# Optimization experiments

Measured on AMD Instinct MI355X. Metric: run time of the kernel, lower is better.

Reference implementation:

```python
import jax, jax.numpy as jnp
import numpy as np

S, L = 512, 32            # number of sequences, max sequence length
IN_FEATURES = 13824       # 512*3*3 + 1024*3*3 ROI features
HID = 1024                # Head.hidden_dim
LSTM_H = HID // 2         # per-direction hidden size (bidirectional)
N_CLASSES = 4787
BN_EPS = 1e-5


def _make_ragged():
    lengths = (4 + (np.arange(S) % 29)).astype(np.int32)  # 4..32, sum = 9121
    n = int(lengths.sum())
    perm = np.random.RandomState(0).permutation(n).astype(np.int32)
    seq_idx = np.zeros((S, L), dtype=np.int32)
    off = 0
    for i, l in enumerate(lengths):
        seq_idx[i, :l] = perm[off:off + l]
        off += l
    return n, jnp.asarray(seq_idx), jnp.asarray(lengths)


def setup_inputs() -> dict:
    n, seq_idx, lengths = _make_ragged()
    key = jax.random.key(0)
    ks = jax.random.split(key, 16)
    w = lambda k, shp, s=0.02: (jax.random.normal(k, shp, dtype=jnp.float32) * s)
    return {
        "x": jax.random.normal(ks[0], (n, IN_FEATURES), dtype=jnp.float32),
        "fc1_w": w(ks[1], (HID, IN_FEATURES)),
        "fc1_b": w(ks[2], (HID,)),
        "bn_gamma": jnp.ones((HID,), jnp.float32),
        "bn_beta": jnp.zeros((HID,), jnp.float32),
        "fc2_w": w(ks[3], (N_CLASSES, HID)),
        "fc2_b": w(ks[4], (N_CLASSES,)),
        "w_ih_f": w(ks[5], (4 * LSTM_H, HID)),
        "w_hh_f": w(ks[6], (4 * LSTM_H, LSTM_H)),
        "b_ih_f": w(ks[7], (4 * LSTM_H,)),
        "b_hh_f": w(ks[8], (4 * LSTM_H,)),
        "w_ih_b": w(ks[9], (4 * LSTM_H, HID)),
        "w_hh_b": w(ks[10], (4 * LSTM_H, LSTM_H)),
        "b_ih_b": w(ks[11], (4 * LSTM_H,)),
        "b_hh_b": w(ks[12], (4 * LSTM_H,)),
        "seq_idx": seq_idx,
        "lengths": lengths,
    }


def _lstm_scan(seq_x, w_ih, w_hh, b_ih, b_hh):
    # seq_x: [S, L, HID] -> outputs [S, L, LSTM_H]; PyTorch gate order i,f,g,o
    s = seq_x.shape[0]
    h0 = jnp.zeros((s, LSTM_H), seq_x.dtype)
    c0 = jnp.zeros((s, LSTM_H), seq_x.dtype)
    x_gates = jnp.einsum('slh,gh->slg', seq_x, w_ih) + b_ih + b_hh  # precompute input gates

    def step(carry, xg):
        h, c = carry
        g = xg + h @ w_hh.T
        i, f, gg, o = jnp.split(g, 4, axis=-1)
        c = jax.nn.sigmoid(f) * c + jax.nn.sigmoid(i) * jnp.tanh(gg)
        h = jax.nn.sigmoid(o) * jnp.tanh(c)
        return (h, c), h

    _, hs = jax.lax.scan(step, (h0, c0), x_gates.transpose(1, 0, 2))  # [L, S, H]
    return hs.transpose(1, 0, 2)


def reference(x, fc1_w, fc1_b, bn_gamma, bn_beta, fc2_w, fc2_b,
              w_ih_f, w_hh_f, b_ih_f, b_hh_f,
              w_ih_b, w_hh_b, b_ih_b, b_hh_b,
              seq_idx, lengths):
    n = x.shape[0]
    # Head: fc1 -> relu -> BatchNorm1d (training-mode batch stats)
    h = jax.nn.relu(x @ fc1_w.T + fc1_b)
    mean = h.mean(axis=0)
    var = jnp.mean((h - mean) ** 2, axis=0)
    feats = (h - mean) * jax.lax.rsqrt(var + BN_EPS) * bn_gamma + bn_beta  # [N, HID]

    # ragged gather into packed [S, L, HID]
    mask = jnp.arange(L)[None, :] < lengths[:, None]          # [S, L]
    gidx = jnp.where(mask, seq_idx, 0)
    seq_x = feats[gidx] * mask[:, :, None]                    # zero padded slots

    # forward direction (padding at tail: harmless to causal scan)
    hf = _lstm_scan(seq_x, w_ih_f, w_hh_f, b_ih_f, b_hh_f)
    # backward direction: reverse each sequence within its valid length
    rev = jnp.clip(lengths[:, None] - 1 - jnp.arange(L)[None, :], 0, L - 1)  # [S, L]
    seq_rev = jnp.take_along_axis(seq_x, rev[:, :, None], axis=1)
    hb_rev = _lstm_scan(seq_rev, w_ih_b, w_hh_b, b_ih_b, b_hh_b)
    hb = jnp.take_along_axis(hb_rev, rev[:, :, None], axis=1)  # un-reverse (involution on valid region)

    out = jnp.concatenate([hf, hb], axis=-1)                   # [S, L, HID]

    # scatter back to flat roi order; padded slots dropped out-of-bounds
    sidx = jnp.where(mask, seq_idx, n).reshape(-1)
    lstm_feats = jnp.zeros((n, HID), feats.dtype).at[sidx].set(
        out.reshape(-1, HID), mode='drop')

    logits = lstm_feats @ fc2_w.T + fc2_b                      # apply_fc_out
    return logits
```

## Files before the change

kernel.cpp:

```cpp
#include <hip/hip_runtime.h>

typedef short short8v __attribute__((ext_vector_type(8)));
typedef float f32x4 __attribute__((ext_vector_type(4)));
typedef _Float16 h4v __attribute__((ext_vector_type(4)));

__device__ __forceinline__ unsigned short f2bf(float f){
  unsigned int u = __float_as_uint(f);
  u += 0x7fffu + ((u >> 16) & 1u);
  return (unsigned short)(u >> 16);
}
__device__ __forceinline__ float bf2f(unsigned short h){
  return __uint_as_float(((unsigned int)h) << 16);
}
union H2F { unsigned short u; _Float16 h; };
__device__ __forceinline__ float fp16f(unsigned short b){ H2F t; t.u = b; return (float)t.h; }

typedef __attribute__((address_space(1))) const unsigned int gu32;
typedef __attribute__((address_space(3))) unsigned int lu32;
__device__ __forceinline__ void gl16(const void* g, void* l){
  __builtin_amdgcn_global_load_lds((gu32*)g, (lu32*)l, 16, 0, 0);
}

template<int EPI>
__global__ __launch_bounds__(512, 2)
void gemm256(const unsigned short* __restrict__ A, const unsigned short* __restrict__ B,
             void* __restrict__ Cout, int M, int N, int K, int lda, int ldb, int ldc,
             const float* __restrict__ bias)
{
  __shared__ __align__(16) unsigned short As[2 * 2 * 256 * 32];
  __shared__ __align__(16) unsigned short Bs[2 * 2 * 256 * 32];

  const int tid = threadIdx.x;
  const int gx = gridDim.x;
  const int nwg = gx * gridDim.y;
  int dd = blockIdx.y * gx + blockIdx.x;
  int q8 = nwg >> 3, r8 = nwg & 7, xc = dd & 7, t8 = dd >> 3;
  int Lid = (xc < r8 ? xc * (q8 + 1) : r8 * (q8 + 1) + (xc - r8) * q8) + t8;
  const int bcol = (Lid % gx) * 256;
  const int brow = (Lid / gx) * 256;

  const int l = tid & 63, w = tid >> 6;
  const int wr = w >> 2;
  const int wn = w & 3;
  const int r16 = l & 15, kg = l >> 4;
  const int swz = (r16 >> 1) & 3;
  const int srow4 = l >> 2, sblk = l & 3;
  const int scol = (sblk ^ ((l >> 3) & 3)) * 8;

  const int kz = blockIdx.z * K;
  const unsigned short* Ag = A + (size_t)(brow + w * 32 + srow4) * lda + kz + scol;
  const unsigned short* Bg = B + (size_t)(bcol + w * 32 + srow4) * ldb + kz + scol;
  unsigned short* Asd = As + w * 1024;
  unsigned short* Bsd = Bs + w * 1024;

#define STA(buf, kh, kt) do { \
    gl16(Ag + (size_t)(kt) * 64 + (kh) * 32, Asd + (buf) * 16384 + (kh) * 8192); \
    gl16(Ag + (size_t)(kt) * 64 + (kh) * 32 + (size_t)16 * lda, Asd + (buf) * 16384 + (kh) * 8192 + 512); \
  } while (0)
#define STB(buf, kh, kt) do { \
    gl16(Bg + (size_t)(kt) * 64 + (kh) * 32, Bsd + (buf) * 16384 + (kh) * 8192); \
    gl16(Bg + (size_t)(kt) * 64 + (kh) * 32 + (size_t)16 * ldb, Bsd + (buf) * 16384 + (kh) * 8192 + 512); \
  } while (0)

  const unsigned short* Ard = As + (wr * 128 + r16) * 32 + ((kg ^ swz) * 8);
  const unsigned short* Brd = Bs + (wn * 64 + r16) * 32 + ((kg ^ swz) * 8);

  f32x4 acc[8][4];
  #pragma unroll
  for (int m = 0; m < 8; m++)
    #pragma unroll
    for (int nn = 0; nn < 4; nn++) { f32x4 z = {0.f, 0.f, 0.f, 0.f}; acc[m][nn] = z; }

  short8v af[4], bfr[4];

#define LDA4(c, kk, mq) { \
    _Pragma("unroll") for (int i = 0; i < 4; i++) \
      af[i] = *(const short8v*)(Ard + (c) * 16384 + (kk) * 8192 + ((mq) * 4 + i) * 512); }
#define LDB4(c, kk) { \
    _Pragma("unroll") for (int nn = 0; nn < 4; nn++) \
      bfr[nn] = *(const short8v*)(Brd + (c) * 16384 + (kk) * 8192 + nn * 512); }
#define MFMAQ(mq) { \
    __builtin_amdgcn_s_setprio(1); \
    _Pragma("unroll") for (int i = 0; i < 4; i++) { \
      _Pragma("unroll") for (int nn = 0; nn < 4; nn++) \
        acc[(mq) * 4 + i][nn] = __builtin_amdgcn_mfma_f32_16x16x32_bf16(af[i], bfr[nn], acc[(mq) * 4 + i][nn], 0, 0, 0); \
    } \
    __builtin_amdgcn_s_setprio(0); }

  const int nk = K >> 6;
  STA(0, 0, 0); STB(0, 0, 0); STA(0, 1, 0); STB(0, 1, 0);
  asm volatile("s_waitcnt vmcnt(4)" ::: "memory");
  __builtin_amdgcn_s_barrier();
  __builtin_amdgcn_sched_barrier(0);

  for (int j = 0; j < nk; j++) {
    const int c = j & 1, nb = c ^ 1;
    const bool pf = (j + 1 < nk);
    LDB4(c, 0); LDA4(c, 0, 0);
    if (pf) STA(nb, 0, j + 1);
    __builtin_amdgcn_s_barrier();
    MFMAQ(0);
    __builtin_amdgcn_s_barrier();
    LDA4(c, 0, 1);
    if (pf) STB(nb, 0, j + 1);
    __builtin_amdgcn_s_barrier();
    MFMAQ(1);
    if (pf) asm volatile("s_waitcnt vmcnt(4)" ::: "memory");
    else    asm volatile("s_waitcnt vmcnt(0)" ::: "memory");
    __builtin_amdgcn_s_barrier();
    __builtin_amdgcn_sched_barrier(0);
    LDB4(c, 1); LDA4(c, 1, 0);
    if (pf) STA(nb, 1, j + 1);
    __builtin_amdgcn_s_barrier();
    MFMAQ(0);
    __builtin_amdgcn_s_barrier();
    LDA4(c, 1, 1);
    if (pf) STB(nb, 1, j + 1);
    __builtin_amdgcn_s_barrier();
    MFMAQ(1);
    if (pf) asm volatile("s_waitcnt vmcnt(4)" ::: "memory");
    __builtin_amdgcn_s_barrier();
    __builtin_amdgcn_sched_barrier(0);
  }
#undef STA
#undef STB
#undef LDA4
#undef LDB4
#undef MFMAQ

  #pragma unroll
  for (int m = 0; m < 8; m++) {
    const int row0 = brow + wr * 128 + m * 16 + kg * 4;
    #pragma unroll
    for (int nn = 0; nn < 4; nn++) {
      const int col = bcol + wn * 64 + nn * 16 + r16;
      if (col < N) {
        const float bv = (EPI == 5) ? 0.f : bias[col];
        #pragma unroll
        for (int rr = 0; rr < 4; rr++) {
          const int row = row0 + rr;
          if (row < M) {
            float val = acc[m][nn][rr] + bv;
            if (EPI == 3) {
              int dL = col >> 11, rc = col & 2047;
              int cg = rc >> 6, g = (rc >> 4) & 3, u = rc & 15;
              int pc = (dL << 11) + (((cg << 4) + u) << 2) + g;
              ((_Float16*)Cout)[(size_t)row * ldc + pc] = (_Float16)val;
            } else if (EPI == 5) {
              ((_Float16*)Cout)[(size_t)blockIdx.z * M * ldc + (size_t)row * ldc + col] = (_Float16)val;
            } else {
              ((float*)Cout)[(size_t)row * ldc + col] = val;
            }
          }
        }
      }
    }
  }
}

__global__ __launch_bounds__(256) void fc1_reduce(const _Float16* __restrict__ P, const float* __restrict__ bias,
                                                  unsigned short* __restrict__ h, float* __restrict__ part,
                                                  int n, int mpad) {
  int b = blockIdx.x, tid = threadIdx.x;
  int c0 = tid * 4;
  float4 bsv = *(const float4*)(bias + c0);
  float s[4] = {0,0,0,0}, qq[4] = {0,0,0,0};
  int rbeg = b * 32;
  for (int r = rbeg; r < rbeg + 32; r++) {
    h4v a0 = *(const h4v*)(P + (size_t)r * 1024 + c0);
    h4v a1 = *(const h4v*)(P + ((size_t)mpad + r) * 1024 + c0);
    h4v a2 = *(const h4v*)(P + ((size_t)2 * mpad + r) * 1024 + c0);
    float v0 = fmaxf((float)a0[0] + (float)a1[0] + (float)a2[0] + bsv.x, 0.f);
    float v1 = fmaxf((float)a0[1] + (float)a1[1] + (float)a2[1] + bsv.y, 0.f);
    float v2 = fmaxf((float)a0[2] + (float)a1[2] + (float)a2[2] + bsv.z, 0.f);
    float v3 = fmaxf((float)a0[3] + (float)a1[3] + (float)a2[3] + bsv.w, 0.f);
    if (r < n) {
      s[0] += v0; qq[0] += v0 * v0;
      s[1] += v1; qq[1] += v1 * v1;
      s[2] += v2; qq[2] += v2 * v2;
      s[3] += v3; qq[3] += v3 * v3;
    }
    *(ushort4*)(h + (size_t)r * 1024 + c0) = make_ushort4(f2bf(v0), f2bf(v1), f2bf(v2), f2bf(v3));
  }
  float* pp = part + (size_t)b * 2048;
  #pragma unroll
  for (int k = 0; k < 4; k++) { pp[(c0 + k) * 2] = s[k]; pp[(c0 + k) * 2 + 1] = qq[k]; }
}

__global__ __launch_bounds__(256, 1)
void lstm_persist(const unsigned short* __restrict__ whhc, const unsigned short* __restrict__ bcp,
                  const _Float16* __restrict__ G,
                  const int* __restrict__ gf, const int* __restrict__ gb, const int* __restrict__ sb,
                  unsigned short* __restrict__ hst,
                  unsigned short* __restrict__ lfeat, int* __restrict__ flags)
{
  __shared__ __align__(16) unsigned short Bsh[128 * 512];
  const int tid = threadIdx.x;
  const int l = tid & 63, w = tid >> 6;
  const int b = blockIdx.x;
  const int grp = b & 15;
  const int c = b >> 4;
  const int d = grp >> 3;
  const int rowbase = d * 512 + (grp & 7) * 64;
  const int r16 = l & 15, kg = l >> 4;
  const int swzl = (r16 & 7) * 8;
  const int hu0 = c * 32 + r16;

  const unsigned short* Bsrc = whhc + ((size_t)(d * 2048 + c * 128)) * 512;
  #pragma unroll
  for (int i = 0; i < 32; i++) {
    int rr = w * 32 + i;
    gl16(Bsrc + (size_t)rr * 512 + ((l * 8) ^ ((rr & 7) * 8)), Bsh + rr * 512);
  }
  asm volatile("s_waitcnt vmcnt(0)");
  __syncthreads();

  float creg[2][4];
  #pragma unroll
  for (int m = 0; m < 2; m++)
    #pragma unroll
    for (int rr = 0; rr < 4; rr++) creg[m][rr] = 0.f;

  const size_t stbase = (size_t)(((grp * 4 + w) * 16 + c) * 4 + (r16 >> 3)) * 128 + (size_t)kg * 32 + (r16 & 7);
  const size_t ldbase = ((size_t)(grp * 64 + w * 16) * 1024) + (size_t)l * 16;

  for (int t = 0; t < 32; t++) {
    ushort4 gv[2][4];
    int scv[4];
    #pragma unroll
    for (int rr = 0; rr < 4; rr++) {
      int row = rowbase + w * 16 + kg * 4 + rr;
      int sq = row & 511;
      int gi = d ? gb[sq * 32 + t] : gf[sq * 32 + t];
      const unsigned short* src = (gi >= 0)
          ? (const unsigned short*)G + ((size_t)gi * 4096 + (d << 11))
          : bcp + (d << 11);
      gv[0][rr] = *(const ushort4*)(src + hu0 * 4);
      gv[1][rr] = *(const ushort4*)(src + (hu0 + 16) * 4);
      scv[rr] = d ? sb[sq * 32 + t] : gi;
    }

    if (t > 0) {
      while (true) {
        int fv = 0x7fffffff;
        if (l < 16)
          fv = __hip_atomic_load(flags + ((grp * 16 + l) << 5), __ATOMIC_RELAXED, __HIP_MEMORY_SCOPE_AGENT);
        if (__all(fv >= t)) break;
        __builtin_amdgcn_s_sleep(1);
      }
    }
    asm volatile("" ::: "memory");

    const unsigned short* hp = hst + (size_t)(t & 1) * 524288;
    unsigned short* hn = hst + (size_t)((t + 1) & 1) * 524288;

    short8v av[16];
    {
      unsigned long long a64 = (unsigned long long)hp * 1 + (unsigned long long)((const char*)0);
      a64 = (unsigned long long)((const char*)hp + ldbase);
      #pragma unroll
      for (int kq = 0; kq < 4; kq++) {
        unsigned long long aq = a64 + (unsigned long long)kq * 4096;
        asm volatile("global_load_dwordx4 %0, %1, off offset:0 sc0 sc1"
                     : "=v"(av[kq * 4 + 0]) : "v"(aq) : "memory");
        asm volatile("global_load_dwordx4 %0, %1, off offset:1024 sc0 sc1"
                     : "=v"(av[kq * 4 + 1]) : "v"(aq) : "memory");
        asm volatile("global_load_dwordx4 %0, %1, off offset:2048 sc0 sc1"
                     : "=v"(av[kq * 4 + 2]) : "v"(aq) : "memory");
        asm volatile("global_load_dwordx4 %0, %1, off offset:3072 sc0 sc1"
                     : "=v"(av[kq * 4 + 3]) : "v"(aq) : "memory");
      }
    }
    asm volatile("s_waitcnt vmcnt(0)" ::: "memory");

    f32x4 acc[8];
    #pragma unroll
    for (int nn = 0; nn < 8; nn++) { f32x4 z = {0.f, 0.f, 0.f, 0.f}; acc[nn] = z; }

    #pragma unroll
    for (int kc = 0; kc < 8; kc++) {
      short8v bv[8][2];
      #pragma unroll
      for (int nn = 0; nn < 8; nn++)
        #pragma unroll
        for (int kk = 0; kk < 2; kk++)
          bv[nn][kk] = *(const short8v*)(Bsh + (nn * 16 + r16) * 512 + ((kc * 64 + kk * 32 + kg * 8) ^ swzl));
      #pragma unroll
      for (int kk = 0; kk < 2; kk++)
        #pragma unroll
        for (int nn = 0; nn < 8; nn++)
          acc[nn] = __builtin_amdgcn_mfma_f32_16x16x32_bf16(av[kc * 2 + kk], bv[nn][kk], acc[nn], 0, 0, 0);
    }

    unsigned long long ha = (unsigned long long)((char*)hn + stbase * 2);
    #pragma unroll
    for (int cgl = 0; cgl < 2; cgl++) {
      const int hu = hu0 + cgl * 16;
      #pragma unroll
      for (int reg = 0; reg < 4; reg++) {
        int row = rowbase + w * 16 + kg * 4 + reg;
        float g_i = acc[cgl * 4 + 0][reg] + fp16f(gv[cgl][reg].x);
        float g_f = acc[cgl * 4 + 1][reg] + fp16f(gv[cgl][reg].y);
        float g_g = acc[cgl * 4 + 2][reg] + fp16f(gv[cgl][reg].z);
        float g_o = acc[cgl * 4 + 3][reg] + fp16f(gv[cgl][reg].w);
        float si = 1.f / (1.f + __expf(-g_i));
        float sf = 1.f / (1.f + __expf(-g_f));
        float so = 1.f / (1.f + __expf(-g_o));
        float cn = sf * creg[cgl][reg] + si * tanhf(g_g);
        float hnv = so * tanhf(cn);
        creg[cgl][reg] = cn;
        unsigned int hb = f2bf(hnv);
        if (cgl == 0) {
          if (reg == 0) asm volatile("global_store_short %0, %1, off offset:0 sc0 sc1" :: "v"(ha), "v"(hb) : "memory");
          if (reg == 1) asm volatile("global_store_short %0, %1, off offset:16 sc0 sc1" :: "v"(ha), "v"(hb) : "memory");
          if (reg == 2) asm volatile("global_store_short %0, %1, off offset:32 sc0 sc1" :: "v"(ha), "v"(hb) : "memory");
          if (reg == 3) asm volatile("global_store_short %0, %1, off offset:48 sc0 sc1" :: "v"(ha), "v"(hb) : "memory");
        } else {
          if (reg == 0) asm volatile("global_store_short %0, %1, off offset:512 sc0 sc1" :: "v"(ha), "v"(hb) : "memory");
          if (reg == 1) asm volatile("global_store_short %0, %1, off offset:528 sc0 sc1" :: "v"(ha), "v"(hb) : "memory");
          if (reg == 2) asm volatile("global_store_short %0, %1, off offset:544 sc0 sc1" :: "v"(ha), "v"(hb) : "memory");
          if (reg == 3) asm volatile("global_store_short %0, %1, off offset:560 sc0 sc1" :: "v"(ha), "v"(hb) : "memory");
        }
        int sc = scv[reg];
        if (sc >= 0) lfeat[(size_t)sc * 1024 + d * 512 + hu] = f2bf(hnv);
      }
    }

    __syncthreads();
    if (t < 31 && tid == 0)
      __hip_atomic_store(flags + ((grp * 16 + c) << 5), t + 1, __ATOMIC_RELAXED, __HIP_MEMORY_SCOPE_AGENT);
  }
}

__global__ __launch_bounds__(256) void conv_bf16(const float* __restrict__ src, unsigned short* __restrict__ dst,
                                                 size_t nvalid, size_t total) {
  size_t stride = (size_t)gridDim.x * 2048;
  for (size_t i = ((size_t)blockIdx.x * 256 + threadIdx.x) * 8; i < total; i += stride) {
    unsigned short o[8];
    if (i + 8 <= nvalid) {
      float4 a = *(const float4*)(src + i);
      float4 b = *(const float4*)(src + i + 4);
      o[0] = f2bf(a.x); o[1] = f2bf(a.y); o[2] = f2bf(a.z); o[3] = f2bf(a.w);
      o[4] = f2bf(b.x); o[5] = f2bf(b.y); o[6] = f2bf(b.z); o[7] = f2bf(b.w);
    } else {
      #pragma unroll
      for (int j = 0; j < 8; j++) o[j] = (i + j < nvalid) ? f2bf(src[i + j]) : (unsigned short)0;
    }
    *(ushort4*)(dst + i) = make_ushort4(o[0], o[1], o[2], o[3]);
    *(ushort4*)(dst + i + 4) = make_ushort4(o[4], o[5], o[6], o[7]);
  }
}

__global__ __launch_bounds__(256) void bn_final(const float* __restrict__ part, const float* __restrict__ gamma,
                                                const float* __restrict__ beta, float* __restrict__ scale,
                                                float* __restrict__ shift, int M, int nb) {
  int c = blockIdx.x * 256 + threadIdx.x;
  float s = 0.f, q = 0.f;
  for (int b = 0; b < nb; b++) { s += part[(size_t)b * 2048 + c * 2]; q += part[(size_t)b * 2048 + c * 2 + 1]; }
  float mean = s / (float)M;
  float var = q / (float)M - mean * mean;
  float sc = gamma[c] * rsqrtf(var + 1e-5f);
  scale[c] = sc; shift[c] = beta[c] - mean * sc;
}

__global__ __launch_bounds__(256) void prep_tables(const int* __restrict__ seq_idx, const int* __restrict__ lengths,
                                                   int* __restrict__ gf, int* __restrict__ gb, int* __restrict__ sb) {
  int idx = blockIdx.x * 256 + threadIdx.x;
  if (idx < 512 * 32) {
    int s = idx >> 5, t = idx & 31;
    int len = lengths[s];
    gf[idx] = (t < len) ? seq_idx[idx] : -1;
    int rb = len - 1 - t;
    gb[idx] = seq_idx[(s << 5) + (rb < 0 ? 0 : rb)];
    sb[idx] = (t < len) ? seq_idx[(s << 5) + (len - 1 - t)] : -1;
  }
}

__global__ __launch_bounds__(256) void build_wih(const float* __restrict__ wf, const float* __restrict__ wb,
                                                 const float* __restrict__ bihf, const float* __restrict__ bhhf,
                                                 const float* __restrict__ bihb, const float* __restrict__ bhhb,
                                                 const float* __restrict__ scale, const float* __restrict__ shift,
                                                 unsigned short* __restrict__ wcdst, float* __restrict__ bc,
                                                 _Float16* __restrict__ bcp) {
  int orow = blockIdx.x * 4 + (threadIdx.x >> 6);
  int l = threadIdx.x & 63;
  int dir = orow >> 11, j = orow & 2047;
  int cc = j >> 6, jj = j & 63, g = jj >> 4, u = jj & 15;
  int srow = g * 512 + cc * 16 + u;
  const float* src = (dir ? wb : wf) + (size_t)srow * 1024;
  unsigned short* dst = wcdst + (size_t)orow * 1024;
  float sacc = 0.f;
  #pragma unroll
  for (int jv = 0; jv < 16; jv++) {
    int k = l + jv * 64;
    float v = src[k];
    sacc += shift[k] * v;
    dst[k] = f2bf(v * scale[k]);
  }
  #pragma unroll
  for (int o2 = 32; o2 > 0; o2 >>= 1) sacc += __shfl_down(sacc, o2);
  if (l == 0) {
    float bb = (dir ? (bihb[srow] + bhhb[srow]) : (bihf[srow] + bhhf[srow])) + sacc;
    bc[orow] = bb;
    int pc = (dir << 11) + (((cc << 4) + u) << 2) + g;
    bcp[pc] = (_Float16)bb;
  }
}

__global__ __launch_bounds__(256) void build_whh(const float* __restrict__ wf, const float* __restrict__ wb,
                                                 unsigned short* __restrict__ o) {
  int cidx = blockIdx.x * 256 + threadIdx.x;
  if (cidx < 4096 * 64) {
    int orow = cidx >> 6, k0 = (cidx & 63) * 8;
    int dir = orow >> 11, j = orow & 2047;
    int cc = j >> 7, L = j & 127;
    int cgl = L >> 6, g = (L >> 4) & 3, u = L & 15;
    int hunit = cc * 32 + cgl * 16 + u;
    const float* src = (dir ? wb : wf) + (size_t)(g * 512 + hunit) * 512 + k0;
    unsigned short* dst = o + (size_t)orow * 512 + k0;
    float4 a = *(const float4*)(src);
    float4 bq = *(const float4*)(src + 4);
    dst[0] = f2bf(a.x); dst[1] = f2bf(a.y); dst[2] = f2bf(a.z); dst[3] = f2bf(a.w);
    dst[4] = f2bf(bq.x); dst[5] = f2bf(bq.y); dst[6] = f2bf(bq.z); dst[7] = f2bf(bq.w);
  }
}

extern "C" void kernel_launch(void* const* d_in, const int* in_sizes, int n_in,
                              void* d_out, int out_size, void* d_ws, size_t ws_size,
                              hipStream_t stream) {
  const float* x     = (const float*)d_in[0];
  const float* fc1w  = (const float*)d_in[1];
  const float* fc1b  = (const float*)d_in[2];
  const float* gamma = (const float*)d_in[3];
  const float* beta  = (const float*)d_in[4];
  const float* fc2w  = (const float*)d_in[5];
  const float* fc2b  = (const float*)d_in[6];
  const float* wihf  = (const float*)d_in[7];
  const float* whhf  = (const float*)d_in[8];
  const float* bihf  = (const float*)d_in[9];
  const float* bhhf  = (const float*)d_in[10];
  const float* wihb  = (const float*)d_in[11];
  const float* whhb  = (const float*)d_in[12];
  const float* bihb  = (const float*)d_in[13];
  const float* bhhb  = (const float*)d_in[14];
  const int* seq_idx = (const int*)d_in[15];
  const int* lengths = (const int*)d_in[16];
  float* out = (float*)d_out;

  const int n = in_sizes[0] / 13824;
  const int mt = (n + 255) / 256;
  const int mpad = mt * 256;

  char* ws = (char*)d_ws;
  size_t off = 0;
  auto alloc = [&](size_t bytes) -> void* {
    void* p = ws + off; off += (bytes + 255) & ~(size_t)255; return p;
  };
  unsigned short* x_h  = (unsigned short*)alloc((size_t)mpad * 13824 * 2);
  unsigned short* w1_h = (unsigned short*)alloc((size_t)1024 * 13824 * 2);
  unsigned short* w2_h = (unsigned short*)alloc((size_t)4864 * 1024 * 2);
  unsigned short* h    = (unsigned short*)alloc((size_t)mpad * 1024 * 2);
  _Float16*       G    = (_Float16*)alloc((size_t)mpad * 4096 * 2);
  unsigned short* wihc = (unsigned short*)alloc((size_t)4096 * 1024 * 2);
  unsigned short* whhc = (unsigned short*)alloc((size_t)4096 * 512 * 2);
  float* bias_c = (float*)alloc(4096 * 4);
  _Float16* bias_p = (_Float16*)alloc(4096 * 2);
  unsigned short* lfeat  = (unsigned short*)alloc((size_t)mpad * 1024 * 2);
  unsigned short* hstate = (unsigned short*)alloc((size_t)2 * 1024 * 512 * 2);
  float* part   = (float*)alloc((size_t)(mpad / 32) * 2048 * 4);
  float* scale  = (float*)alloc(1024 * 4);
  float* shift  = (float*)alloc(1024 * 4);
  int* gf  = (int*)alloc(16384 * 4);
  int* gb  = (int*)alloc(16384 * 4);
  int* sb  = (int*)alloc(16384 * 4);
  int* flags = (int*)alloc(256 * 32 * 4);

  _Float16* P16 = (_Float16*)G;

  dim3 blk(256);
  dim3 blk5(512);

  conv_bf16<<<2048, blk, 0, stream>>>(x, x_h, (size_t)n * 13824, (size_t)mpad * 13824);
  conv_bf16<<<1024, blk, 0, stream>>>(fc1w, w1_h, (size_t)1024 * 13824, (size_t)1024 * 13824);
  conv_bf16<<<256, blk, 0, stream>>>(fc2w, w2_h, (size_t)4787 * 1024, (size_t)4864 * 1024);
  build_whh<<<1024, blk, 0, stream>>>(whhf, whhb, whhc);
  prep_tables<<<64, blk, 0, stream>>>(seq_idx, lengths, gf, gb, sb);
  hipMemsetAsync(hstate, 0, (size_t)2 * 1024 * 512 * 2, stream);
  hipMemsetAsync(flags, 0, 256 * 32 * 4, stream);

  gemm256<5><<<dim3(4, mt, 3), blk5, 0, stream>>>(
      x_h, w1_h, P16, mpad, 1024, 4608, 13824, 13824, 1024, nullptr);

  fc1_reduce<<<mpad / 32, blk, 0, stream>>>(P16, fc1b, h, part, n, mpad);
  bn_final<<<4, blk, 0, stream>>>(part, gamma, beta, scale, shift, n, mpad / 32);
  build_wih<<<1024, blk, 0, stream>>>(wihf, wihb, bihf, bhhf, bihb, bhhb, scale, shift, wihc, bias_c, bias_p);

  gemm256<3><<<dim3(16, mt), blk5, 0, stream>>>(
      h, wihc, G, n, 4096, 1024, 1024, 1024, 4096, bias_c);

  lstm_persist<<<256, blk, 0, stream>>>(whhc, (const unsigned short*)bias_p, G, gf, gb, sb,
                                        hstate, lfeat, flags);

  gemm256<0><<<dim3(19, mt), blk5, 0, stream>>>(
      lfeat, w2_h, out, n, 4787, 1024, 1024, 1024, 4787, fc2b);
}
```

Measured before the change: 1.135 ms.

## Simplify GEMM main loop to issue all prefetches then one MFMA block

After: 1.197 ms. +5.4%, slower.

```diff
diff --git a/kernel.cpp b/kernel.cpp
--- a/kernel.cpp
+++ b/kernel.cpp
@@ -71,62 +71,51 @@
     #pragma unroll
     for (int nn = 0; nn < 4; nn++) { f32x4 z = {0.f, 0.f, 0.f, 0.f}; acc[m][nn] = z; }
 
-  short8v af[4], bfr[4];
-
-#define LDA4(c, kk, mq) { \
-    _Pragma("unroll") for (int i = 0; i < 4; i++) \
-      af[i] = *(const short8v*)(Ard + (c) * 16384 + (kk) * 8192 + ((mq) * 4 + i) * 512); }
-#define LDB4(c, kk) { \
-    _Pragma("unroll") for (int nn = 0; nn < 4; nn++) \
-      bfr[nn] = *(const short8v*)(Brd + (c) * 16384 + (kk) * 8192 + nn * 512); }
-#define MFMAQ(mq) { \
-    __builtin_amdgcn_s_setprio(1); \
-    _Pragma("unroll") for (int i = 0; i < 4; i++) { \
-      _Pragma("unroll") for (int nn = 0; nn < 4; nn++) \
-        acc[(mq) * 4 + i][nn] = __builtin_amdgcn_mfma_f32_16x16x32_bf16(af[i], bfr[nn], acc[(mq) * 4 + i][nn], 0, 0, 0); \
-    } \
-    __builtin_amdgcn_s_setprio(0); }
-
   const int nk = K >> 6;
   STA(0, 0, 0); STB(0, 0, 0); STA(0, 1, 0); STB(0, 1, 0);
-  asm volatile("s_waitcnt vmcnt(4)" ::: "memory");
+  asm volatile("s_waitcnt vmcnt(0)" ::: "memory");
   __builtin_amdgcn_s_barrier();
   __builtin_amdgcn_sched_barrier(0);
 
   for (int j = 0; j < nk; j++) {
     const int c = j & 1, nb = c ^ 1;
     const bool pf = (j + 1 < nk);
-    LDB4(c, 0); LDA4(c, 0, 0);
-    if (pf) STA(nb, 0, j + 1);
-    __builtin_amdgcn_s_barrier();
-    MFMAQ(0);
-    __builtin_amdgcn_s_barrier();
-    LDA4(c, 0, 1);
-    if (pf) STB(nb, 0, j + 1);
-    __builtin_amdgcn_s_barrier();
-    MFMAQ(1);
-    if (pf) asm volatile("s_waitcnt vmcnt(4)" ::: "memory");
-    else    asm volatile("s_waitcnt vmcnt(0)" ::: "memory");
+    if (pf) { STA(nb, 0, j + 1); STB(nb, 0, j + 1); STA(nb, 1, j + 1); STB(nb, 1, j + 1); }
+
+    short8v afr[2][2][4];
+    short8v bfr2[2][4];
+    #pragma unroll
+    for (int kh = 0; kh < 2; kh++) {
+      #pragma unroll
+      for (int nn = 0; nn < 4; nn++)
+        bfr2[kh][nn] = *(const short8v*)(Brd + c * 16384 + kh * 8192 + nn * 512);
+      #pragma unroll
+      for (int mq = 0; mq < 2; mq++)
+        #pragma unroll
+        for (int i = 0; i < 4; i++)
+          afr[kh][mq][i] = *(const short8v*)(Ard + c * 16384 + kh * 8192 + (mq * 4 + i) * 512);
+    }
+
+    __builtin_amdgcn_s_setprio(1);
+    #pragma unroll
+    for (int kh = 0; kh < 2; kh++)
+      #pragma unroll
+      for (int mq = 0; mq < 2; mq++)
+        #pragma unroll
+        for (int i = 0; i < 4; i++)
+          #pragma unroll
+          for (int nn = 0; nn < 4; nn++)
+            acc[mq * 4 + i][nn] = __builtin_amdgcn_mfma_f32_16x16x32_bf16(
+                afr[kh][mq][i], bfr2[kh][nn], acc[mq * 4 + i][nn], 0, 0, 0);
+    __builtin_amdgcn_s_setprio(0);
+    __builtin_amdgcn_sched_barrier(0);
+
+    asm volatile("s_waitcnt vmcnt(0)" ::: "memory");
     __builtin_amdgcn_s_barrier();
     __builtin_amdgcn_sched_barrier(0);
-    LDB4(c, 1); LDA4(c, 1, 0);
-    if (pf) STA(nb, 1, j + 1);
-    __builtin_amdgcn_s_barrier();
-    MFMAQ(0);
-    __builtin_amdgcn_s_barrier();
-    LDA4(c, 1, 1);
-    if (pf) STB(nb, 1, j + 1);
-    __builtin_amdgcn_s_barrier();
-    MFMAQ(1);
-    if (pf) asm volatile("s_waitcnt vmcnt(4)" ::: "memory");
-    __builtin_amdgcn_s_barrier();
-    __builtin_amdgcn_sched_barrier(0);
   }
 #undef STA
 #undef STB
-#undef LDA4
-#undef LDB4
-#undef MFMAQ
 
   #pragma unroll
   for (int m = 0; m < 8; m++) {
@@ -256,8 +245,7 @@
 
     short8v av[16];
     {
-      unsigned long long a64 = (unsigned long long)hp * 1 + (unsigned long long)((const char*)0);
-      a64 = (unsigned long long)((const char*)hp + ldbase);
+      unsigned long long a64 = (unsigned long long)((const char*)hp + ldbase);
       #pragma unroll
       for (int kq = 0; kq < 4; kq++) {
         unsigned long long aq = a64 + (unsigned long long)kq * 4096;
```

## Fuse fp32-to-bf16 conversion of x into fc1 GEMM A-tile loading

Applied to the files above, without the earlier changes.

Result: faster. 1.087 ms (-4.3%).

```diff
diff --git a/kernel.cpp b/kernel.cpp
--- a/kernel.cpp
+++ b/kernel.cpp
@@ -124,9 +124,6 @@
   }
 #undef STA
 #undef STB
-#undef LDA4
-#undef LDB4
-#undef MFMAQ
 
   #pragma unroll
   for (int m = 0; m < 8; m++) {
@@ -135,7 +132,7 @@
     for (int nn = 0; nn < 4; nn++) {
       const int col = bcol + wn * 64 + nn * 16 + r16;
       if (col < N) {
-        const float bv = (EPI == 5) ? 0.f : bias[col];
+        const float bv = bias[col];
         #pragma unroll
         for (int rr = 0; rr < 4; rr++) {
           const int row = row0 + rr;
@@ -146,12 +143,167 @@
               int cg = rc >> 6, g = (rc >> 4) & 3, u = rc & 15;
               int pc = (dL << 11) + (((cg << 4) + u) << 2) + g;
               ((_Float16*)Cout)[(size_t)row * ldc + pc] = (_Float16)val;
-            } else if (EPI == 5) {
-              ((_Float16*)Cout)[(size_t)blockIdx.z * M * ldc + (size_t)row * ldc + col] = (_Float16)val;
             } else {
               ((float*)Cout)[(size_t)row * ldc + col] = val;
             }
           }
+        }
+      }
+    }
+  }
+}
+
+__global__ __launch_bounds__(512, 2)
+void gemm256fA(const float* __restrict__ A, const unsigned short* __restrict__ B,
+               _Float16* __restrict__ Cout, int M, int N, int K, int lda, int ldb, int ldc,
+               int nvalid)
+{
+  __shared__ __align__(16) unsigned short As[2 * 2 * 256 * 32];
+  __shared__ __align__(16) unsigned short Bs[2 * 2 * 256 * 32];
+
+  const int tid = threadIdx.x;
+  const int gx = gridDim.x;
+  const int nwg = gx * gridDim.y;
+  int dd = blockIdx.y * gx + blockIdx.x;
+  int q8 = nwg >> 3, r8 = nwg & 7, xc = dd & 7, t8 = dd >> 3;
+  int Lid = (xc < r8 ? xc * (q8 + 1) : r8 * (q8 + 1) + (xc - r8) * q8) + t8;
+  const int bcol = (Lid % gx) * 256;
+  const int brow = (Lid / gx) * 256;
+
+  const int l = tid & 63, w = tid >> 6;
+  const int wr = w >> 2;
+  const int wn = w & 3;
+  const int r16 = l & 15, kg = l >> 4;
+  const int swz = (r16 >> 1) & 3;
+  const int srow4 = l >> 2, sblk = l & 3;
+  const int scol = (sblk ^ ((l >> 3) & 3)) * 8;
+
+  const int kz = blockIdx.z * K;
+  const unsigned short* Bg = B + (size_t)(bcol + w * 32 + srow4) * ldb + kz + scol;
+  unsigned short* Bsd = Bs + w * 1024;
+
+#define STB(buf, kh, kt) do { \
+    gl16(Bg + (size_t)(kt) * 64 + (kh) * 32, Bsd + (buf) * 16384 + (kh) * 8192); \
+    gl16(Bg + (size_t)(kt) * 64 + (kh) * 32 + (size_t)16 * ldb, Bsd + (buf) * 16384 + (kh) * 8192 + 512); \
+  } while (0)
+
+  const int rsel = l >> 4;
+  const int kb16 = l & 15;
+  const int khA  = kb16 >> 3;
+  const int gA   = (kb16 >> 1) & 3;
+  const int hfA  = kb16 & 1;
+  unsigned long long abase[8];
+  int dstA[8];
+  #pragma unroll
+  for (int i = 0; i < 8; i++) {
+    int rowA = brow + w * 32 + i * 4 + rsel;
+    if (rowA >= nvalid) rowA = nvalid - 1;
+    abase[i] = (unsigned long long)(A + (size_t)rowA * lda + kz) + (unsigned long long)kb16 * 16;
+    int row_local = w * 32 + i * 4 + rsel;
+    int swi = (row_local >> 1) & 3;
+    dstA[i] = khA * 8192 + row_local * 32 + ((gA ^ swi) * 8) + hfA * 4;
+  }
+
+  const unsigned short* Ard = As + (wr * 128 + r16) * 32 + ((kg ^ swz) * 8);
+  const unsigned short* Brd = Bs + (wn * 64 + r16) * 32 + ((kg ^ swz) * 8);
+
+  f32x4 acc[8][4];
+  #pragma unroll
+  for (int m = 0; m < 8; m++)
+    #pragma unroll
+    for (int nn = 0; nn < 4; nn++) { f32x4 z = {0.f, 0.f, 0.f, 0.f}; acc[m][nn] = z; }
+
+  short8v af[4], bfr[4];
+  f32x4 ar[8];
+
+#define ALOAD(kt) { \
+    _Pragma("unroll") for (int i = 0; i < 8; i++) { \
+      unsigned long long aq = abase[i] + (unsigned long long)(kt) * 256; \
+      asm volatile("global_load_dwordx4 %0, %1, off" : "=v"(ar[i]) : "v"(aq) : "memory"); \
+    } }
+#define AWRITE(buf) { \
+    _Pragma("unroll") for (int i = 0; i < 8; i++) { \
+      unsigned int lo_, hi_; \
+      asm("v_cvt_pk_bf16_f32 %0, %1, %2" : "=v"(lo_) : "v"(ar[i][0]), "v"(ar[i][1])); \
+      asm("v_cvt_pk_bf16_f32 %0, %1, %2" : "=v"(hi_) : "v"(ar[i][2]), "v"(ar[i][3])); \
+      uint2 pv_; pv_.x = lo_; pv_.y = hi_; \
+      *(uint2*)(As + (buf) * 16384 + dstA[i]) = pv_; \
+    } }
+
+  const int nk = K >> 6;
+  ALOAD(0);
+  STB(0, 0, 0); STB(0, 1, 0);
+  asm volatile("s_waitcnt vmcnt(4)" ::: "memory");
+  __builtin_amdgcn_sched_barrier(0);
+  AWRITE(0);
+  asm volatile("s_waitcnt vmcnt(0) lgkmcnt(0)" ::: "memory");
+  __builtin_amdgcn_s_barrier();
+  __builtin_amdgcn_sched_barrier(0);
+
+#define LDA4(c, kk, mq) { \
+    _Pragma("unroll") for (int i = 0; i < 4; i++) \
+      af[i] = *(const short8v*)(Ard + (c) * 16384 + (kk) * 8192 + ((mq) * 4 + i) * 512); }
+#define LDB4(c, kk) { \
+    _Pragma("unroll") for (int nn = 0; nn < 4; nn++) \
+      bfr[nn] = *(const short8v*)(Brd + (c) * 16384 + (kk) * 8192 + nn * 512); }
+#define MFMAQ(mq) { \
+    __builtin_amdgcn_s_setprio(1); \
+    _Pragma("unroll") for (int i = 0; i < 4; i++) { \
+      _Pragma("unroll") for (int nn = 0; nn < 4; nn++) \
+        acc[(mq) * 4 + i][nn] = __builtin_amdgcn_mfma_f32_16x16x32_bf16(af[i], bfr[nn], acc[(mq) * 4 + i][nn], 0, 0, 0); \
+    } \
+    __builtin_amdgcn_s_setprio(0); }
+
+  for (int j = 0; j < nk; j++) {
+    const int c = j & 1, nb = c ^ 1;
+    const bool pf = (j + 1 < nk);
+    LDB4(c, 0); LDA4(c, 0, 0);
+    if (pf) ALOAD(j + 1);
+    __builtin_amdgcn_s_barrier();
+    MFMAQ(0);
+    __builtin_amdgcn_s_barrier();
+    LDA4(c, 0, 1);
+    if (pf) STB(nb, 0, j + 1);
+    __builtin_amdgcn_s_barrier();
+    MFMAQ(1);
+    __builtin_amdgcn_s_barrier();
+    __builtin_amdgcn_sched_barrier(0);
+    LDB4(c, 1); LDA4(c, 1, 0);
+    if (pf) {
+      asm volatile("s_waitcnt vmcnt(2)" ::: "memory");
+      __builtin_amdgcn_sched_barrier(0);
+      AWRITE(nb);
+      STB(nb, 1, j + 1);
+    }
+    __builtin_amdgcn_s_barrier();
+    MFMAQ(0);
+    __builtin_amdgcn_s_barrier();
+    LDA4(c, 1, 1);
+    __builtin_amdgcn_s_barrier();
+    MFMAQ(1);
+    asm volatile("s_waitcnt vmcnt(0) lgkmcnt(0)" ::: "memory");
+    __builtin_amdgcn_s_barrier();
+    __builtin_amdgcn_sched_barrier(0);
+  }
+#undef STB
+#undef ALOAD
+#undef AWRITE
+#undef LDA4
+#undef LDB4
+#undef MFMAQ
+
+  #pragma unroll
+  for (int m = 0; m < 8; m++) {
+    const int row0 = brow + wr * 128 + m * 16 + kg * 4;
+    #pragma unroll
+    for (int nn = 0; nn < 4; nn++) {
+      const int col = bcol + wn * 64 + nn * 16 + r16;
+      if (col < N) {
+        #pragma unroll
+        for (int rr = 0; rr < 4; rr++) {
+          const int row = row0 + rr;
+          if (row < M)
+            Cout[(size_t)blockIdx.z * M * ldc + (size_t)row * ldc + col] = (_Float16)(acc[m][nn][rr]);
         }
       }
     }
@@ -256,8 +408,7 @@
 
     short8v av[16];
     {
-      unsigned long long a64 = (unsigned long long)hp * 1 + (unsigned long long)((const char*)0);
-      a64 = (unsigned long long)((const char*)hp + ldbase);
+      unsigned long long a64 = (unsigned long long)((const char*)hp + ldbase);
       #pragma unroll
       for (int kq = 0; kq < 4; kq++) {
         unsigned long long aq = a64 + (unsigned long long)kq * 4096;
@@ -298,7 +449,6 @@
       const int hu = hu0 + cgl * 16;
       #pragma unroll
       for (int reg = 0; reg < 4; reg++) {
-        int row = rowbase + w * 16 + kg * 4 + reg;
         float g_i = acc[cgl * 4 + 0][reg] + fp16f(gv[cgl][reg].x);
         float g_f = acc[cgl * 4 + 1][reg] + fp16f(gv[cgl][reg].y);
         float g_g = acc[cgl * 4 + 2][reg] + fp16f(gv[cgl][reg].z);
@@ -456,7 +606,6 @@
   auto alloc = [&](size_t bytes) -> void* {
     void* p = ws + off; off += (bytes + 255) & ~(size_t)255; return p;
   };
-  unsigned short* x_h  = (unsigned short*)alloc((size_t)mpad * 13824 * 2);
   unsigned short* w1_h = (unsigned short*)alloc((size_t)1024 * 13824 * 2);
   unsigned short* w2_h = (unsigned short*)alloc((size_t)4864 * 1024 * 2);
   unsigned short* h    = (unsigned short*)alloc((size_t)mpad * 1024 * 2);
@@ -480,7 +629,6 @@
   dim3 blk(256);
   dim3 blk5(512);
 
-  conv_bf16<<<2048, blk, 0, stream>>>(x, x_h, (size_t)n * 13824, (size_t)mpad * 13824);
   conv_bf16<<<1024, blk, 0, stream>>>(fc1w, w1_h, (size_t)1024 * 13824, (size_t)1024 * 13824);
   conv_bf16<<<256, blk, 0, stream>>>(fc2w, w2_h, (size_t)4787 * 1024, (size_t)4864 * 1024);
   build_whh<<<1024, blk, 0, stream>>>(whhf, whhb, whhc);
@@ -488,8 +636,8 @@
   hipMemsetAsync(hstate, 0, (size_t)2 * 1024 * 512 * 2, stream);
   hipMemsetAsync(flags, 0, 256 * 32 * 4, stream);
 
-  gemm256<5><<<dim3(4, mt, 3), blk5, 0, stream>>>(
-      x_h, w1_h, P16, mpad, 1024, 4608, 13824, 13824, 1024, nullptr);
+  gemm256fA<<<dim3(4, mt, 3), blk5, 0, stream>>>(
+      x, w1_h, P16, mpad, 1024, 4608, 13824, 13824, 1024, n);
 
   fc1_reduce<<<mpad / 32, blk, 0, stream>>>(P16, fc1b, h, part, n, mpad);
   bn_final<<<4, blk, 0, stream>>>(part, gamma, beta, scale, shift, n, mpad / 32);
```
